# Kernel optimization log

Measured on AMD Instinct MI355X. Metric: run time of the kernel, lower is better.

The kernel has to match this reference:

```python
import jax, jax.numpy as jnp
import numpy as np

B, S, D = 16, 4096, 64


def setup_inputs() -> dict:
    key = jax.random.key(0)
    kq, kk, kv = jax.random.split(key, 3)
    q = jax.random.normal(kq, (B, S, D), dtype=jnp.float32)
    k = jax.random.normal(kk, (B, S, D), dtype=jnp.float32)
    v = jax.random.normal(kv, (B, S, D), dtype=jnp.float32)
    inv_scale_factor = jnp.float32(1.0 / np.sqrt(D))  # source DIVIDES by this
    p = 0  # dropout prob (deterministic baseline -> identity)
    return {"q": q, "k": k, "v": v, "inv_scale_factor": inv_scale_factor, "p": p}


def reference(q, k, v, inv_scale_factor, p):
    # qk = q @ k^T ; scaled = qk / inv_scale_factor (faithful to source)
    scores = jnp.einsum("bsd,btd->bst", q, k) / inv_scale_factor  # [B,S,S]
    attn = jax.nn.softmax(scores, axis=-1)
    # dropout with p=0 is identity (eval-mode baseline)
    out = jnp.einsum("bst,btd->bsd", attn, v)  # [B,S,D]
    return out
```

## Files before the change

### kernel.cpp

```cpp
#include <hip/hip_runtime.h>
#include <hip/hip_bf16.h>

typedef float f32x4 __attribute__((ext_vector_type(4)));
typedef float f32x16 __attribute__((ext_vector_type(16)));
typedef _Float16 half8 __attribute__((ext_vector_type(8)));
typedef __bf16 bf16x8 __attribute__((ext_vector_type(8)));
typedef __bf16 bf16x4 __attribute__((ext_vector_type(4)));
typedef unsigned short ushort_t;

constexpr int Bb = 16, Ss = 4096, Dd = 64;
constexpr int KBLK = 32, QBLK = 128;
constexpr int NT = Ss / KBLK;
constexpr float kLOG2E = 1.44269504088896340736f;
constexpr float DEFER_THR = 10.0f;

constexpr int KP_BLOCKS = (Bb * Ss * Dd / 8) / 256;
constexpr int VT_BLOCKS = (Bb * Dd * (Ss / 32)) / 256;

#define GLOAD_LDS16(gp, lp)                                                              \
    __builtin_amdgcn_global_load_lds(                                                    \
        (const __attribute__((address_space(1))) void*)(gp),                             \
        (__attribute__((address_space(3))) void*)(lp), 16, 0, 0)

__global__ __launch_bounds__(256)
void prep_f16s(const float* __restrict__ K, const float* __restrict__ V,
               _Float16* __restrict__ Khi, _Float16* __restrict__ Klo,
               _Float16* __restrict__ Vt)
{
    const int bid = blockIdx.x;
    if (bid < KP_BLOCKS) {
        const size_t idx = ((size_t)bid * 256 + threadIdx.x) * 8;
        const float4 a = *reinterpret_cast<const float4*>(K + idx);
        const float4 c = *reinterpret_cast<const float4*>(K + idx + 4);
        float xs[8] = {a.x, a.y, a.z, a.w, c.x, c.y, c.z, c.w};
        half8 h8, l8;
#pragma unroll
        for (int i = 0; i < 8; ++i) {
            const _Float16 h = (_Float16)xs[i];
            h8[i] = h;
            l8[i] = (_Float16)(xs[i] - (float)h);
        }
        *reinterpret_cast<half8*>(Khi + idx) = h8;
        *reinterpret_cast<half8*>(Klo + idx) = l8;
    } else {
        const int t = (bid - KP_BLOCKS) * 256 + threadIdx.x;
        const int d = t & 63;
        const int s32 = (t >> 6) & (Ss / 32 - 1);
        const int b = t >> 13;
        const float* vp = V + ((size_t)b * Ss + (size_t)s32 * 32) * Dd + d;
        __align__(16) _Float16 ob[32];
#pragma unroll
        for (int j = 0; j < 32; ++j) ob[j] = (_Float16)vp[(size_t)j * Dd];
        _Float16* op = Vt + ((size_t)b * Dd + d) * Ss + (size_t)s32 * 32;
#pragma unroll
        for (int j8 = 0; j8 < 4; ++j8)
            *reinterpret_cast<half8*>(op + j8 * 8) = *reinterpret_cast<half8*>(ob + j8 * 8);
    }
}

__global__ __launch_bounds__(512, 4)
void attn_fwd_v5(const float* __restrict__ Q, const float* __restrict__ inv_scale,
                 const _Float16* __restrict__ Khi, const _Float16* __restrict__ Klo,
                 const _Float16* __restrict__ Vt, float* __restrict__ Out)
{
    __shared__ __align__(16) unsigned char smem[48 * 1024];

    const int tid = threadIdx.x;
    const int lane = tid & 63;
    const int w = tid >> 6;
    const int p = w & 1;
    const int qg = w >> 1;
    const int l31 = lane & 31;
    const int hi = lane >> 5;

    const int bid = (blockIdx.x & 7) * 64 + (blockIdx.x >> 3);
    const int b = bid >> 5;
    const int q0 = (bid & 31) * QBLK;

    const _Float16* KhB = Khi + (size_t)b * Ss * Dd;
    const _Float16* KlB = Klo + (size_t)b * Ss * Dd;
    const _Float16* VB = Vt + (size_t)b * Dd * Ss;

    const int c = tid & 255;
    const int kk = c >> 3;
    const int ksrc = kk * Dd + (((c & 7) ^ (kk & 7)) << 3);
    const int dd_ = c >> 2;
    const size_t vsrc = (size_t)dd_ * Ss + (((c & 3) ^ (dd_ & 3)) << 3);

#define STAGE(t)                                                                            \
    do {                                                                                    \
        const int _sl = (t) & 3;                                                            \
        if (tid < 256) {                                                                    \
            GLOAD_LDS16(KhB + (size_t)(t) * (KBLK * Dd) + ksrc,                             \
                        smem + _sl * 4096 + c * 16);                                        \
            GLOAD_LDS16(KlB + (size_t)(t) * (KBLK * Dd) + ksrc,                             \
                        smem + 16384 + _sl * 4096 + c * 16);                                \
        } else {                                                                            \
            GLOAD_LDS16(VB + (size_t)(t) * KBLK + vsrc,                                     \
                        smem + 32768 + _sl * 4096 + c * 16);                                \
        }                                                                                   \
    } while (0)

    STAGE(0);
    STAGE(1);

    int koff[4], voff[4];
#pragma unroll
    for (int ks = 0; ks < 4; ++ks)
        koff[ks] = l31 * 128 + ((((ks << 1) + hi) ^ (l31 & 7)) << 4);
#pragma unroll
    for (int i = 0; i < 4; ++i) {
        const int d = (i >> 1) * 32 + l31;
        voff[i] = d * 64 + (((((i & 1) << 1) + hi) ^ (d & 3)) << 4);
    }

    union H8 { half8 h; unsigned int u[4]; };
    H8 qhi[4], qlo[4];
    {
        const float s2 = (1.0f / inv_scale[0]) * kLOG2E;
        const float* qrow = Q + ((size_t)b * Ss + q0 + qg * 32 + l31) * Dd;
#pragma unroll
        for (int ks = 0; ks < 4; ++ks) {
            const int d0 = ks * 16 + hi * 8;
            const float4 a = *reinterpret_cast<const float4*>(qrow + d0);
            const float4 cc = *reinterpret_cast<const float4*>(qrow + d0 + 4);
            float xs[8] = {a.x, a.y, a.z, a.w, cc.x, cc.y, cc.z, cc.w};
#pragma unroll
            for (int i = 0; i < 8; ++i) {
                const float x = xs[i] * s2;
                const _Float16 h = (_Float16)x;
                qhi[ks].h[i] = h;
                qlo[ks].h[i] = (_Float16)(x - (float)h);
            }
        }
    }

    f32x16 O0, O1;
#pragma unroll
    for (int r = 0; r < 16; ++r) { O0[r] = 0.f; O1[r] = 0.f; }
    float m_run = -INFINITY, l_run = 0.f;

    __syncthreads();

    for (int it = 0; it < NT / 2; ++it) {
        const int t = 2 * it + p;
        const unsigned char* khbase = smem + (t & 3) * 4096;
        const unsigned char* klbase = smem + 16384 + (t & 3) * 4096;
        const unsigned char* vbase = smem + 32768 + (t & 3) * 4096;

        if (it < NT / 2 - 1) { STAGE(2 * it + 2); STAGE(2 * it + 3); }

        f32x16 S;
#pragma unroll
        for (int r = 0; r < 16; ++r) S[r] = 0.f;
#pragma unroll
        for (int ks = 0; ks < 4; ++ks) {
            const half8 kh = *reinterpret_cast<const half8*>(khbase + koff[ks]);
            const half8 kl = *reinterpret_cast<const half8*>(klbase + koff[ks]);
            S = __builtin_amdgcn_mfma_f32_32x32x16_f16(kh, qhi[ks].h, S, 0, 0, 0);
            S = __builtin_amdgcn_mfma_f32_32x32x16_f16(kl, qhi[ks].h, S, 0, 0, 0);
            S = __builtin_amdgcn_mfma_f32_32x32x16_f16(kh, qlo[ks].h, S, 0, 0, 0);
        }

        float tmax = S[0];
#pragma unroll
        for (int r = 1; r < 16; ++r) tmax = fmaxf(tmax, S[r]);
        tmax = fmaxf(tmax, __shfl_xor(tmax, 32));

        float fac = 1.0f;
        if (__any(tmax > m_run + DEFER_THR)) {
            const float m_new = fmaxf(m_run, tmax);
            fac = __builtin_amdgcn_exp2f(m_run - m_new);
            m_run = m_new;
#pragma unroll
            for (int r = 0; r < 16; ++r) { O0[r] *= fac; O1[r] *= fac; }
        }

        float tsum = 0.f;
#pragma unroll
        for (int r = 0; r < 16; ++r) {
            S[r] = __builtin_amdgcn_exp2f(S[r] - m_run);
            tsum += S[r];
        }
        tsum += __shfl_xor(tsum, 32);
        l_run = l_run * fac + tsum;

        unsigned int wd[8];
#pragma unroll
        for (int j = 0; j < 8; ++j) {
            const auto h2 = __builtin_amdgcn_cvt_pkrtz(S[2 * j], S[2 * j + 1]);
            wd[j] = __builtin_bit_cast(unsigned int, h2);
        }
        auto xhalf = [&](unsigned int& a, unsigned int& cx) {
            const unsigned int y = hi ? a : cx;
            const unsigned int sy = __shfl_xor(y, 32);
            const unsigned int na = hi ? sy : a;
            const unsigned int nc = hi ? cx : sy;
            a = na; cx = nc;
        };
        xhalf(wd[0], wd[2]);
        xhalf(wd[1], wd[3]);
        xhalf(wd[4], wd[6]);
        xhalf(wd[5], wd[7]);

        H8 pf0, pf1;
        pf0.u[0] = wd[0]; pf0.u[1] = wd[1]; pf0.u[2] = wd[2]; pf0.u[3] = wd[3];
        pf1.u[0] = wd[4]; pf1.u[1] = wd[5]; pf1.u[2] = wd[6]; pf1.u[3] = wd[7];

        O0 = __builtin_amdgcn_mfma_f32_32x32x16_f16(
            *reinterpret_cast<const half8*>(vbase + voff[0]), pf0.h, O0, 0, 0, 0);
        O0 = __builtin_amdgcn_mfma_f32_32x32x16_f16(
            *reinterpret_cast<const half8*>(vbase + voff[1]), pf1.h, O0, 0, 0, 0);
        O1 = __builtin_amdgcn_mfma_f32_32x32x16_f16(
            *reinterpret_cast<const half8*>(vbase + voff[2]), pf0.h, O1, 0, 0, 0);
        O1 = __builtin_amdgcn_mfma_f32_32x32x16_f16(
            *reinterpret_cast<const half8*>(vbase + voff[3]), pf1.h, O1, 0, 0, 0);

        __syncthreads();
    }

    float* mO = (float*)smem;
    float* ml = (float*)(smem + 32768);

    if (p == 1) {
#pragma unroll
        for (int dblk = 0; dblk < 2; ++dblk)
#pragma unroll
            for (int rr = 0; rr < 4; ++rr) {
                f32x4 v;
                if (dblk == 0) {
                    v[0] = O0[rr * 4 + 0]; v[1] = O0[rr * 4 + 1];
                    v[2] = O0[rr * 4 + 2]; v[3] = O0[rr * 4 + 3];
                } else {
                    v[0] = O1[rr * 4 + 0]; v[1] = O1[rr * 4 + 1];
                    v[2] = O1[rr * 4 + 2]; v[3] = O1[rr * 4 + 3];
                }
                *reinterpret_cast<f32x4*>(mO + (((qg * 2 + dblk) * 4 + rr) << 8) + lane * 4) = v;
            }
        if (hi == 0) {
            ml[qg * 64 + l31] = m_run;
            ml[qg * 64 + 32 + l31] = l_run;
        }
    }
    __syncthreads();
    if (p == 0) {
        const float m1 = ml[qg * 64 + l31];
        const float l1 = ml[qg * 64 + 32 + l31];
        const float mm = fmaxf(m_run, m1);
        float f0 = __builtin_amdgcn_exp2f(m_run - mm);
        float f1 = __builtin_amdgcn_exp2f(m1 - mm);
        const float inv = 1.0f / (l_run * f0 + l1 * f1);
        f0 *= inv; f1 *= inv;
        float* orow = Out + ((size_t)b * Ss + q0 + qg * 32 + l31) * Dd;
#pragma unroll
        for (int dblk = 0; dblk < 2; ++dblk)
#pragma unroll
            for (int rr = 0; rr < 4; ++rr) {
                const f32x4 ov = *reinterpret_cast<const f32x4*>(
                    mO + (((qg * 2 + dblk) * 4 + rr) << 8) + lane * 4);
                f32x4 res;
#pragma unroll
                for (int j = 0; j < 4; ++j) {
                    const float mine = (dblk == 0) ? O0[rr * 4 + j] : O1[rr * 4 + j];
                    res[j] = mine * f0 + ov[j] * f1;
                }
                *reinterpret_cast<f32x4*>(orow + dblk * 32 + rr * 8 + hi * 4) = res;
            }
    }
#undef STAGE
}

__global__ __launch_bounds__(256)
void attn_fwd_fallback(const float* __restrict__ Q, const float* __restrict__ K,
                       const float* __restrict__ V, const float* __restrict__ inv_scale,
                       float* __restrict__ Out)
{
    __shared__ __align__(16) ushort_t sKhi[KBLK * Dd];
    __shared__ __align__(16) ushort_t sKlo[KBLK * Dd];
    __shared__ __align__(16) ushort_t sVt[Dd * KBLK];
    __shared__ __align__(16) ushort_t sP[4][16 * KBLK];

    const int tid = threadIdx.x;
    const int lane = tid & 63;
    const int w = tid >> 6;
    const int q15 = lane & 15;
    const int g = lane >> 4;
    const int b = blockIdx.x >> 6;
    const int q0 = (blockIdx.x & 63) * 64;
    const float scale = 1.0f / inv_scale[0];

    const float* qptr = Q + (((size_t)b * Ss) + q0 + w * 16 + q15) * Dd;
    bf16x8 qhi[2], qlo[2];
#pragma unroll
    for (int ds = 0; ds < 2; ++ds) {
        const float4 f0 = *reinterpret_cast<const float4*>(qptr + ds * 32 + g * 8);
        const float4 f1 = *reinterpret_cast<const float4*>(qptr + ds * 32 + g * 8 + 4);
        float xs[8] = {f0.x, f0.y, f0.z, f0.w, f1.x, f1.y, f1.z, f1.w};
#pragma unroll
        for (int i = 0; i < 8; ++i) {
            __bf16 h = (__bf16)xs[i];
            qhi[ds][i] = h;
            qlo[ds][i] = (__bf16)(xs[i] - (float)h);
        }
    }
    const int krs = tid >> 3;
    const int kc8 = (tid & 7) * 8;
    const int kidx = krs * Dd + (kc8 ^ ((krs & 7) << 3));
    const float* kbase = K + ((size_t)b * Ss) * Dd;
    const int vd = tid & 63;
    const int vk8 = (tid >> 6) * 8;
    const int vidx = vd * KBLK + (vk8 ^ ((vd & 3) << 3));
    const float* vbase = V + ((size_t)b * Ss) * Dd;

    f32x4 Oacc[4];
#pragma unroll
    for (int dt = 0; dt < 4; ++dt)
#pragma unroll
        for (int r = 0; r < 4; ++r) Oacc[dt][r] = 0.f;
    float m_run = -INFINITY, l_run = 0.f;

    for (int k0 = 0; k0 < Ss; k0 += KBLK) {
        {
            const float* p0 = kbase + (size_t)(k0 + krs) * Dd + kc8;
            const float4 a = *reinterpret_cast<const float4*>(p0);
            const float4 c = *reinterpret_cast<const float4*>(p0 + 4);
            float xs[8] = {a.x, a.y, a.z, a.w, c.x, c.y, c.z, c.w};
            bf16x8 h8, l8;
#pragma unroll
            for (int i = 0; i < 8; ++i) {
                __bf16 h = (__bf16)xs[i];
                h8[i] = h;
                l8[i] = (__bf16)(xs[i] - (float)h);
            }
            *reinterpret_cast<bf16x8*>(&sKhi[kidx]) = h8;
            *reinterpret_cast<bf16x8*>(&sKlo[kidx]) = l8;
        }
        {
            bf16x8 v8;
#pragma unroll
            for (int j = 0; j < 8; ++j) v8[j] = (__bf16)vbase[(size_t)(k0 + vk8 + j) * Dd + vd];
            *reinterpret_cast<bf16x8*>(&sVt[vidx]) = v8;
        }
        __syncthreads();

        float z[2][4];
#pragma unroll
        for (int t = 0; t < 2; ++t) {
            const int krow = t * 16 + q15;
            f32x4 acc;
            acc[0] = acc[1] = acc[2] = acc[3] = 0.f;
#pragma unroll
            for (int ds = 0; ds < 2; ++ds) {
                const int ci = (ds * 32 + g * 8) ^ ((krow & 7) << 3);
                const bf16x8 kh = *reinterpret_cast<const bf16x8*>(&sKhi[krow * Dd + ci]);
                const bf16x8 kl = *reinterpret_cast<const bf16x8*>(&sKlo[krow * Dd + ci]);
                acc = __builtin_amdgcn_mfma_f32_16x16x32_bf16(kh, qhi[ds], acc, 0, 0, 0);
                acc = __builtin_amdgcn_mfma_f32_16x16x32_bf16(kl, qhi[ds], acc, 0, 0, 0);
                acc = __builtin_amdgcn_mfma_f32_16x16x32_bf16(kh, qlo[ds], acc, 0, 0, 0);
            }
#pragma unroll
            for (int r = 0; r < 4; ++r) z[t][r] = acc[r] * scale;
        }

        float tmax = z[0][0];
#pragma unroll
        for (int t = 0; t < 2; ++t)
#pragma unroll
            for (int r = 0; r < 4; ++r) tmax = fmaxf(tmax, z[t][r]);
        tmax = fmaxf(tmax, __shfl_xor(tmax, 16));
        tmax = fmaxf(tmax, __shfl_xor(tmax, 32));
        const float m_new = fmaxf(m_run, tmax);

        float pz[2][4];
        float tsum = 0.f;
#pragma unroll
        for (int t = 0; t < 2; ++t)
#pragma unroll
            for (int r = 0; r < 4; ++r) {
                const float e = __builtin_amdgcn_exp2f((z[t][r] - m_new) * kLOG2E);
                pz[t][r] = e;
                tsum += e;
            }
        tsum += __shfl_xor(tsum, 16);
        tsum += __shfl_xor(tsum, 32);
        const float fac = __builtin_amdgcn_exp2f((m_run - m_new) * kLOG2E);
        l_run = l_run * fac + tsum;
        m_run = m_new;

#pragma unroll
        for (int t = 0; t < 2; ++t) {
            bf16x4 pb;
#pragma unroll
            for (int r = 0; r < 4; ++r) pb[r] = (__bf16)pz[t][r];
            const int pidx = q15 * KBLK + ((t * 16 + g * 4) ^ ((q15 & 3) << 3));
            *reinterpret_cast<bf16x4*>(&sP[w][pidx]) = pb;
        }
        {
            const float fr0 = __shfl(fac, g * 4 + 0);
            const float fr1 = __shfl(fac, g * 4 + 1);
            const float fr2 = __shfl(fac, g * 4 + 2);
            const float fr3 = __shfl(fac, g * 4 + 3);
#pragma unroll
            for (int dt = 0; dt < 4; ++dt) {
                Oacc[dt][0] *= fr0; Oacc[dt][1] *= fr1;
                Oacc[dt][2] *= fr2; Oacc[dt][3] *= fr3;
            }
        }
        const int paidx = q15 * KBLK + ((g * 8) ^ ((q15 & 3) << 3));
        const bf16x8 pa = *reinterpret_cast<const bf16x8*>(&sP[w][paidx]);
#pragma unroll
        for (int dt = 0; dt < 4; ++dt) {
            const int dd = dt * 16 + q15;
            const bf16x8 vf =
                *reinterpret_cast<const bf16x8*>(&sVt[dd * KBLK + ((g * 8) ^ ((dd & 3) << 3))]);
            Oacc[dt] = __builtin_amdgcn_mfma_f32_16x16x32_bf16(pa, vf, Oacc[dt], 0, 0, 0);
        }
        __syncthreads();
    }

    const float invl = 1.0f / l_run;
    float il[4];
#pragma unroll
    for (int r = 0; r < 4; ++r) il[r] = __shfl(invl, g * 4 + r);
    float* obase = Out + (((size_t)b * Ss) + q0 + w * 16) * Dd;
#pragma unroll
    for (int dt = 0; dt < 4; ++dt)
#pragma unroll
        for (int r = 0; r < 4; ++r)
            obase[(size_t)(g * 4 + r) * Dd + dt * 16 + q15] = Oacc[dt][r] * il[r];
}

extern "C" void kernel_launch(void* const* d_in, const int* in_sizes, int n_in,
                              void* d_out, int out_size, void* d_ws, size_t ws_size,
                              hipStream_t stream)
{
    const float* q = (const float*)d_in[0];
    const float* k = (const float*)d_in[1];
    const float* v = (const float*)d_in[2];
    const float* inv_scale = (const float*)d_in[3];
    float* out = (float*)d_out;
    (void)in_sizes; (void)n_in; (void)out_size;

    const size_t NKV = (size_t)Bb * Ss * Dd;
    const size_t need = NKV * 3 * sizeof(_Float16);

    if (ws_size >= need) {
        _Float16* Khi = (_Float16*)d_ws;
        _Float16* Klo = Khi + NKV;
        _Float16* Vt = Klo + NKV;
        hipLaunchKernelGGL(prep_f16s, dim3(KP_BLOCKS + VT_BLOCKS), dim3(256), 0, stream,
                           k, v, Khi, Klo, Vt);
        hipLaunchKernelGGL(attn_fwd_v5, dim3(Bb * (Ss / QBLK)), dim3(512), 0, stream,
                           q, inv_scale, Khi, Klo, Vt, out);
    } else {
        hipLaunchKernelGGL(attn_fwd_fallback, dim3(Bb * 64), dim3(256), 0, stream,
                           q, k, v, inv_scale, out);
    }
}
```

Baseline: 170.5 us.

## Software-pipeline QK^T of next tile with softmax and PV of previous tile

Restructures the main loop so each iteration issues the QK^T MFMAs for the next key tile into one score buffer while running softmax and PV on the previous tile's scores held in a second buffer. V staging grows to eight LDS slots (64 KB shared memory) so V stays resident one tile longer, and the V swizzle is changed to a different XOR pattern. It also raises wave priority around the MFMA sections. The aim is to hide exp/shuffle latency behind matrix work, at the cost of more registers and more LDS, which may reduce occupancy.

Measured after the change: 178.4 us. +4.7%, slower.

```diff
diff --git a/kernel.cpp b/kernel.cpp
--- a/kernel.cpp
+++ b/kernel.cpp
@@ -58,12 +58,14 @@
     }
 }
 
+union H8 { half8 h; unsigned int u[4]; };
+
 __global__ __launch_bounds__(512, 4)
-void attn_fwd_v5(const float* __restrict__ Q, const float* __restrict__ inv_scale,
+void attn_fwd_v6(const float* __restrict__ Q, const float* __restrict__ inv_scale,
                  const _Float16* __restrict__ Khi, const _Float16* __restrict__ Klo,
                  const _Float16* __restrict__ Vt, float* __restrict__ Out)
 {
-    __shared__ __align__(16) unsigned char smem[48 * 1024];
+    __shared__ __align__(16) unsigned char smem[64 * 1024];
 
     const int tid = threadIdx.x;
     const int lane = tid & 63;
@@ -85,19 +87,18 @@
     const int kk = c >> 3;
     const int ksrc = kk * Dd + (((c & 7) ^ (kk & 7)) << 3);
     const int dd_ = c >> 2;
-    const size_t vsrc = (size_t)dd_ * Ss + (((c & 3) ^ (dd_ & 3)) << 3);
+    const size_t vsrc = (size_t)dd_ * Ss + (((c & 3) ^ ((dd_ >> 1) & 3)) << 3);
 
 #define STAGE(t)                                                                            \
     do {                                                                                    \
-        const int _sl = (t) & 3;                                                            \
         if (tid < 256) {                                                                    \
             GLOAD_LDS16(KhB + (size_t)(t) * (KBLK * Dd) + ksrc,                             \
-                        smem + _sl * 4096 + c * 16);                                        \
+                        smem + ((t) & 3) * 4096 + c * 16);                                  \
             GLOAD_LDS16(KlB + (size_t)(t) * (KBLK * Dd) + ksrc,                             \
-                        smem + 16384 + _sl * 4096 + c * 16);                                \
+                        smem + 16384 + ((t) & 3) * 4096 + c * 16);                          \
         } else {                                                                            \
             GLOAD_LDS16(VB + (size_t)(t) * KBLK + vsrc,                                     \
-                        smem + 32768 + _sl * 4096 + c * 16);                                \
+                        smem + 32768 + ((t) & 7) * 4096 + c * 16);                          \
         }                                                                                   \
     } while (0)
 
@@ -111,10 +112,9 @@
 #pragma unroll
     for (int i = 0; i < 4; ++i) {
         const int d = (i >> 1) * 32 + l31;
-        voff[i] = d * 64 + (((((i & 1) << 1) + hi) ^ (d & 3)) << 4);
-    }
-
-    union H8 { half8 h; unsigned int u[4]; };
+        voff[i] = d * 64 + (((((i & 1) << 1) + hi) ^ ((d >> 1) & 3)) << 4);
+    }
+
     H8 qhi[4], qlo[4];
     {
         const float s2 = (1.0f / inv_scale[0]) * kLOG2E;
@@ -135,89 +135,103 @@
         }
     }
 
-    f32x16 O0, O1;
-#pragma unroll
-    for (int r = 0; r < 16; ++r) { O0[r] = 0.f; O1[r] = 0.f; }
+    f32x16 Sa, Sb, O0, O1;
+#pragma unroll
+    for (int r = 0; r < 16; ++r) { O0[r] = 0.f; O1[r] = 0.f; Sa[r] = 0.f; Sb[r] = 0.f; }
     float m_run = -INFINITY, l_run = 0.f;
 
+    auto xhalf = [&](unsigned int& a, unsigned int& cx) {
+        const unsigned int y = hi ? a : cx;
+        const unsigned int sy = __shfl_xor(y, 32);
+        const unsigned int na = hi ? sy : a;
+        const unsigned int nc = hi ? cx : sy;
+        a = na; cx = nc;
+    };
+
+#define QK_STEP(IT, SQK)                                                                   \
+    do {                                                                                   \
+        const int _tq = 2 * (IT) + p;                                                      \
+        const unsigned char* _khb = smem + (_tq & 3) * 4096;                               \
+        const unsigned char* _klb = smem + 16384 + (_tq & 3) * 4096;                       \
+        _Pragma("unroll") for (int r = 0; r < 16; ++r) SQK[r] = 0.f;                       \
+        __builtin_amdgcn_s_setprio(1);                                                     \
+        _Pragma("unroll") for (int ks = 0; ks < 4; ++ks) {                                 \
+            const half8 _kh = *reinterpret_cast<const half8*>(_khb + koff[ks]);            \
+            const half8 _kl = *reinterpret_cast<const half8*>(_klb + koff[ks]);            \
+            SQK = __builtin_amdgcn_mfma_f32_32x32x16_f16(_kh, qhi[ks].h, SQK, 0, 0, 0);    \
+            SQK = __builtin_amdgcn_mfma_f32_32x32x16_f16(_kl, qhi[ks].h, SQK, 0, 0, 0);    \
+            SQK = __builtin_amdgcn_mfma_f32_32x32x16_f16(_kh, qlo[ks].h, SQK, 0, 0, 0);    \
+        }                                                                                  \
+        __builtin_amdgcn_s_setprio(0);                                                     \
+    } while (0)
+
+#define SM_PV(TP, SSM)                                                                     \
+    do {                                                                                   \
+        float _tmax = SSM[0];                                                              \
+        _Pragma("unroll") for (int r = 1; r < 16; ++r) _tmax = fmaxf(_tmax, SSM[r]);       \
+        _tmax = fmaxf(_tmax, __shfl_xor(_tmax, 32));                                       \
+        float _fac = 1.0f;                                                                 \
+        if (__any(_tmax > m_run + DEFER_THR)) {                                            \
+            const float _mn = fmaxf(m_run, _tmax);                                         \
+            _fac = __builtin_amdgcn_exp2f(m_run - _mn);                                    \
+            m_run = _mn;                                                                   \
+            _Pragma("unroll") for (int r = 0; r < 16; ++r) { O0[r] *= _fac; O1[r] *= _fac; } \
+        }                                                                                  \
+        float _tsum = 0.f;                                                                 \
+        _Pragma("unroll") for (int r = 0; r < 16; ++r) {                                   \
+            SSM[r] = __builtin_amdgcn_exp2f(SSM[r] - m_run);                               \
+            _tsum += SSM[r];                                                               \
+        }                                                                                  \
+        _tsum += __shfl_xor(_tsum, 32);                                                    \
+        l_run = l_run * _fac + _tsum;                                                      \
+        unsigned int _wd[8];                                                               \
+        _Pragma("unroll") for (int j = 0; j < 8; ++j) {                                    \
+            const auto _h2 = __builtin_amdgcn_cvt_pkrtz(SSM[2 * j], SSM[2 * j + 1]);       \
+            _wd[j] = __builtin_bit_cast(unsigned int, _h2);                                \
+        }                                                                                  \
+        xhalf(_wd[0], _wd[2]); xhalf(_wd[1], _wd[3]);                                      \
+        xhalf(_wd[4], _wd[6]); xhalf(_wd[5], _wd[7]);                                      \
+        H8 _pf0, _pf1;                                                                     \
+        _pf0.u[0] = _wd[0]; _pf0.u[1] = _wd[1]; _pf0.u[2] = _wd[2]; _pf0.u[3] = _wd[3];    \
+        _pf1.u[0] = _wd[4]; _pf1.u[1] = _wd[5]; _pf1.u[2] = _wd[6]; _pf1.u[3] = _wd[7];    \
+        const unsigned char* _vb = smem + 32768 + ((TP) & 7) * 4096;                       \
+        __builtin_amdgcn_s_setprio(1);                                                     \
+        O0 = __builtin_amdgcn_mfma_f32_32x32x16_f16(                                       \
+            *reinterpret_cast<const half8*>(_vb + voff[0]), _pf0.h, O0, 0, 0, 0);          \
+        O0 = __builtin_amdgcn_mfma_f32_32x32x16_f16(                                       \
+            *reinterpret_cast<const half8*>(_vb + voff[1]), _pf1.h, O0, 0, 0, 0);          \
+        O1 = __builtin_amdgcn_mfma_f32_32x32x16_f16(                                       \
+            *reinterpret_cast<const half8*>(_vb + voff[2]), _pf0.h, O1, 0, 0, 0);          \
+        O1 = __builtin_amdgcn_mfma_f32_32x32x16_f16(                                       \
+            *reinterpret_cast<const half8*>(_vb + voff[3]), _pf1.h, O1, 0, 0, 0);          \
+        __builtin_amdgcn_s_setprio(0);                                                     \
+    } while (0)
+
     __syncthreads();
 
-    for (int it = 0; it < NT / 2; ++it) {
-        const int t = 2 * it + p;
-        const unsigned char* khbase = smem + (t & 3) * 4096;
-        const unsigned char* klbase = smem + 16384 + (t & 3) * 4096;
-        const unsigned char* vbase = smem + 32768 + (t & 3) * 4096;
-
-        if (it < NT / 2 - 1) { STAGE(2 * it + 2); STAGE(2 * it + 3); }
-
-        f32x16 S;
-#pragma unroll
-        for (int r = 0; r < 16; ++r) S[r] = 0.f;
-#pragma unroll
-        for (int ks = 0; ks < 4; ++ks) {
-            const half8 kh = *reinterpret_cast<const half8*>(khbase + koff[ks]);
-            const half8 kl = *reinterpret_cast<const half8*>(klbase + koff[ks]);
-            S = __builtin_amdgcn_mfma_f32_32x32x16_f16(kh, qhi[ks].h, S, 0, 0, 0);
-            S = __builtin_amdgcn_mfma_f32_32x32x16_f16(kl, qhi[ks].h, S, 0, 0, 0);
-            S = __builtin_amdgcn_mfma_f32_32x32x16_f16(kh, qlo[ks].h, S, 0, 0, 0);
-        }
-
-        float tmax = S[0];
-#pragma unroll
-        for (int r = 1; r < 16; ++r) tmax = fmaxf(tmax, S[r]);
-        tmax = fmaxf(tmax, __shfl_xor(tmax, 32));
-
-        float fac = 1.0f;
-        if (__any(tmax > m_run + DEFER_THR)) {
-            const float m_new = fmaxf(m_run, tmax);
-            fac = __builtin_amdgcn_exp2f(m_run - m_new);
-            m_run = m_new;
-#pragma unroll
-            for (int r = 0; r < 16; ++r) { O0[r] *= fac; O1[r] *= fac; }
-        }
-
-        float tsum = 0.f;
-#pragma unroll
-        for (int r = 0; r < 16; ++r) {
-            S[r] = __builtin_amdgcn_exp2f(S[r] - m_run);
-            tsum += S[r];
-        }
-        tsum += __shfl_xor(tsum, 32);
-        l_run = l_run * fac + tsum;
-
-        unsigned int wd[8];
-#pragma unroll
-        for (int j = 0; j < 8; ++j) {
-            const auto h2 = __builtin_amdgcn_cvt_pkrtz(S[2 * j], S[2 * j + 1]);
-            wd[j] = __builtin_bit_cast(unsigned int, h2);
-        }
-        auto xhalf = [&](unsigned int& a, unsigned int& cx) {
-            const unsigned int y = hi ? a : cx;
-            const unsigned int sy = __shfl_xor(y, 32);
-            const unsigned int na = hi ? sy : a;
-            const unsigned int nc = hi ? cx : sy;
-            a = na; cx = nc;
-        };
-        xhalf(wd[0], wd[2]);
-        xhalf(wd[1], wd[3]);
-        xhalf(wd[4], wd[6]);
-        xhalf(wd[5], wd[7]);
-
-        H8 pf0, pf1;
-        pf0.u[0] = wd[0]; pf0.u[1] = wd[1]; pf0.u[2] = wd[2]; pf0.u[3] = wd[3];
-        pf1.u[0] = wd[4]; pf1.u[1] = wd[5]; pf1.u[2] = wd[6]; pf1.u[3] = wd[7];
-
-        O0 = __builtin_amdgcn_mfma_f32_32x32x16_f16(
-            *reinterpret_cast<const half8*>(vbase + voff[0]), pf0.h, O0, 0, 0, 0);
-        O0 = __builtin_amdgcn_mfma_f32_32x32x16_f16(
-            *reinterpret_cast<const half8*>(vbase + voff[1]), pf1.h, O0, 0, 0, 0);
-        O1 = __builtin_amdgcn_mfma_f32_32x32x16_f16(
-            *reinterpret_cast<const half8*>(vbase + voff[2]), pf0.h, O1, 0, 0, 0);
-        O1 = __builtin_amdgcn_mfma_f32_32x32x16_f16(
-            *reinterpret_cast<const half8*>(vbase + voff[3]), pf1.h, O1, 0, 0, 0);
-
+    STAGE(2); STAGE(3);
+    QK_STEP(0, Sa);
+    __syncthreads();
+
+    for (int ih = 0; ih < 31; ++ih) {
+        const int itA = 2 * ih + 1;
+        STAGE(2 * itA + 2); STAGE(2 * itA + 3);
+        QK_STEP(itA, Sb);
+        SM_PV(2 * itA - 2 + p, Sa);
         __syncthreads();
-    }
+
+        const int itB = 2 * ih + 2;
+        STAGE(2 * itB + 2); STAGE(2 * itB + 3);
+        QK_STEP(itB, Sa);
+        SM_PV(2 * itB - 2 + p, Sb);
+        __syncthreads();
+    }
+
+    QK_STEP(63, Sb);
+    SM_PV(124 + p, Sa);
+    __syncthreads();
+
+    SM_PV(126 + p, Sb);
 
     float* mO = (float*)smem;
     float* ml = (float*)(smem + 32768);
@@ -268,6 +282,8 @@
             }
     }
 #undef STAGE
+#undef QK_STEP
+#undef SM_PV
 }
 
 __global__ __launch_bounds__(256)
@@ -450,7 +466,7 @@
         _Float16* Vt = Klo + NKV;
         hipLaunchKernelGGL(prep_f16s, dim3(KP_BLOCKS + VT_BLOCKS), dim3(256), 0, stream,
                            k, v, Khi, Klo, Vt);
-        hipLaunchKernelGGL(attn_fwd_v5, dim3(Bb * (Ss / QBLK)), dim3(512), 0, stream,
+        hipLaunchKernelGGL(attn_fwd_v6, dim3(Bb * (Ss / QBLK)), dim3(512), 0, stream,
                            q, inv_scale, Khi, Klo, Vt, out);
     } else {
         hipLaunchKernelGGL(attn_fwd_fallback, dim3(Bb * 64), dim3(256), 0, stream,
```

## Give each wave two query sub-tiles to reuse K/V fragments with half the threads

Applied to the files above, without the earlier changes.

Shrinks the attention block from 512 to 256 threads. Each wave now processes two 32-row query sub-tiles, so every K and V fragment read from LDS feeds two MFMA chains instead of one, halving LDS reads per MFMA. All threads now issue the K-hi, K-lo and V async loads, the V swizzle pattern is changed, and s_setprio is raised around the MFMA bursts. The cost is doubled accumulator and score registers, which lowers occupancy, plus an epilogue merge that runs twice in sequence.

Result: slower. 175.5 us (+3.0%).

```diff
diff --git a/kernel.cpp b/kernel.cpp
--- a/kernel.cpp
+++ b/kernel.cpp
@@ -58,10 +58,12 @@
     }
 }
 
-__global__ __launch_bounds__(512, 4)
-void attn_fwd_v5(const float* __restrict__ Q, const float* __restrict__ inv_scale,
-                 const _Float16* __restrict__ Khi, const _Float16* __restrict__ Klo,
-                 const _Float16* __restrict__ Vt, float* __restrict__ Out)
+union H8 { half8 h; unsigned int u[4]; };
+
+__global__ __launch_bounds__(256, 2)
+void attn_fwd_v10(const float* __restrict__ Q, const float* __restrict__ inv_scale,
+                  const _Float16* __restrict__ Khi, const _Float16* __restrict__ Klo,
+                  const _Float16* __restrict__ Vt, float* __restrict__ Out)
 {
     __shared__ __align__(16) unsigned char smem[48 * 1024];
 
@@ -81,24 +83,19 @@
     const _Float16* KlB = Klo + (size_t)b * Ss * Dd;
     const _Float16* VB = Vt + (size_t)b * Dd * Ss;
 
-    const int c = tid & 255;
-    const int kk = c >> 3;
-    const int ksrc = kk * Dd + (((c & 7) ^ (kk & 7)) << 3);
-    const int dd_ = c >> 2;
-    const size_t vsrc = (size_t)dd_ * Ss + (((c & 3) ^ (dd_ & 3)) << 3);
+    const int kk = tid >> 3;
+    const int ksrc = kk * Dd + (((tid & 7) ^ (kk & 7)) << 3);
+    const int dd_ = tid >> 2;
+    const size_t vsrc = (size_t)dd_ * Ss + (((tid & 3) ^ ((dd_ >> 1) & 3)) << 3);
 
 #define STAGE(t)                                                                            \
     do {                                                                                    \
-        const int _sl = (t) & 3;                                                            \
-        if (tid < 256) {                                                                    \
-            GLOAD_LDS16(KhB + (size_t)(t) * (KBLK * Dd) + ksrc,                             \
-                        smem + _sl * 4096 + c * 16);                                        \
-            GLOAD_LDS16(KlB + (size_t)(t) * (KBLK * Dd) + ksrc,                             \
-                        smem + 16384 + _sl * 4096 + c * 16);                                \
-        } else {                                                                            \
-            GLOAD_LDS16(VB + (size_t)(t) * KBLK + vsrc,                                     \
-                        smem + 32768 + _sl * 4096 + c * 16);                                \
-        }                                                                                   \
+        GLOAD_LDS16(KhB + (size_t)(t) * (KBLK * Dd) + ksrc,                                 \
+                    smem + ((t) & 3) * 4096 + tid * 16);                                    \
+        GLOAD_LDS16(KlB + (size_t)(t) * (KBLK * Dd) + ksrc,                                 \
+                    smem + 16384 + ((t) & 3) * 4096 + tid * 16);                            \
+        GLOAD_LDS16(VB + (size_t)(t) * KBLK + vsrc,                                         \
+                    smem + 32768 + ((t) & 3) * 4096 + tid * 16);                            \
     } while (0)
 
     STAGE(0);
@@ -111,34 +108,45 @@
 #pragma unroll
     for (int i = 0; i < 4; ++i) {
         const int d = (i >> 1) * 32 + l31;
-        voff[i] = d * 64 + (((((i & 1) << 1) + hi) ^ (d & 3)) << 4);
-    }
-
-    union H8 { half8 h; unsigned int u[4]; };
-    H8 qhi[4], qlo[4];
+        voff[i] = d * 64 + (((((i & 1) << 1) + hi) ^ ((d >> 1) & 3)) << 4);
+    }
+
+    H8 qhi[2][4], qlo[2][4];
     {
         const float s2 = (1.0f / inv_scale[0]) * kLOG2E;
-        const float* qrow = Q + ((size_t)b * Ss + q0 + qg * 32 + l31) * Dd;
-#pragma unroll
-        for (int ks = 0; ks < 4; ++ks) {
-            const int d0 = ks * 16 + hi * 8;
-            const float4 a = *reinterpret_cast<const float4*>(qrow + d0);
-            const float4 cc = *reinterpret_cast<const float4*>(qrow + d0 + 4);
-            float xs[8] = {a.x, a.y, a.z, a.w, cc.x, cc.y, cc.z, cc.w};
-#pragma unroll
-            for (int i = 0; i < 8; ++i) {
-                const float x = xs[i] * s2;
-                const _Float16 h = (_Float16)x;
-                qhi[ks].h[i] = h;
-                qlo[ks].h[i] = (_Float16)(x - (float)h);
-            }
-        }
-    }
-
-    f32x16 O0, O1;
-#pragma unroll
-    for (int r = 0; r < 16; ++r) { O0[r] = 0.f; O1[r] = 0.f; }
-    float m_run = -INFINITY, l_run = 0.f;
+#pragma unroll
+        for (int qs = 0; qs < 2; ++qs) {
+            const float* qrow =
+                Q + ((size_t)b * Ss + q0 + qg * 64 + qs * 32 + l31) * Dd;
+#pragma unroll
+            for (int ks = 0; ks < 4; ++ks) {
+                const int d0 = ks * 16 + hi * 8;
+                const float4 a = *reinterpret_cast<const float4*>(qrow + d0);
+                const float4 cc = *reinterpret_cast<const float4*>(qrow + d0 + 4);
+                float xs[8] = {a.x, a.y, a.z, a.w, cc.x, cc.y, cc.z, cc.w};
+#pragma unroll
+                for (int i = 0; i < 8; ++i) {
+                    const float x = xs[i] * s2;
+                    const _Float16 h = (_Float16)x;
+                    qhi[qs][ks].h[i] = h;
+                    qlo[qs][ks].h[i] = (_Float16)(x - (float)h);
+                }
+            }
+        }
+    }
+
+    f32x16 O0, O1, O2, O3;
+#pragma unroll
+    for (int r = 0; r < 16; ++r) { O0[r] = 0.f; O1[r] = 0.f; O2[r] = 0.f; O3[r] = 0.f; }
+    float m0 = -INFINITY, l0 = 0.f, m1 = -INFINITY, l1 = 0.f;
+
+    auto xhalf = [&](unsigned int& a, unsigned int& cx) {
+        const unsigned int y = hi ? a : cx;
+        const unsigned int sy = __shfl_xor(y, 32);
+        const unsigned int na = hi ? sy : a;
+        const unsigned int nc = hi ? cx : sy;
+        a = na; cx = nc;
+    };
 
     __syncthreads();
 
@@ -150,123 +158,146 @@
 
         if (it < NT / 2 - 1) { STAGE(2 * it + 2); STAGE(2 * it + 3); }
 
-        f32x16 S;
-#pragma unroll
-        for (int r = 0; r < 16; ++r) S[r] = 0.f;
+        f32x16 S0, S1;
+#pragma unroll
+        for (int r = 0; r < 16; ++r) { S0[r] = 0.f; S1[r] = 0.f; }
+        __builtin_amdgcn_s_setprio(1);
 #pragma unroll
         for (int ks = 0; ks < 4; ++ks) {
             const half8 kh = *reinterpret_cast<const half8*>(khbase + koff[ks]);
             const half8 kl = *reinterpret_cast<const half8*>(klbase + koff[ks]);
-            S = __builtin_amdgcn_mfma_f32_32x32x16_f16(kh, qhi[ks].h, S, 0, 0, 0);
-            S = __builtin_amdgcn_mfma_f32_32x32x16_f16(kl, qhi[ks].h, S, 0, 0, 0);
-            S = __builtin_amdgcn_mfma_f32_32x32x16_f16(kh, qlo[ks].h, S, 0, 0, 0);
-        }
-
-        float tmax = S[0];
-#pragma unroll
-        for (int r = 1; r < 16; ++r) tmax = fmaxf(tmax, S[r]);
-        tmax = fmaxf(tmax, __shfl_xor(tmax, 32));
-
-        float fac = 1.0f;
-        if (__any(tmax > m_run + DEFER_THR)) {
-            const float m_new = fmaxf(m_run, tmax);
-            fac = __builtin_amdgcn_exp2f(m_run - m_new);
-            m_run = m_new;
-#pragma unroll
-            for (int r = 0; r < 16; ++r) { O0[r] *= fac; O1[r] *= fac; }
-        }
-
-        float tsum = 0.f;
+            S0 = __builtin_amdgcn_mfma_f32_32x32x16_f16(kh, qhi[0][ks].h, S0, 0, 0, 0);
+            S1 = __builtin_amdgcn_mfma_f32_32x32x16_f16(kh, qhi[1][ks].h, S1, 0, 0, 0);
+            S0 = __builtin_amdgcn_mfma_f32_32x32x16_f16(kl, qhi[0][ks].h, S0, 0, 0, 0);
+            S1 = __builtin_amdgcn_mfma_f32_32x32x16_f16(kl, qhi[1][ks].h, S1, 0, 0, 0);
+            S0 = __builtin_amdgcn_mfma_f32_32x32x16_f16(kh, qlo[0][ks].h, S0, 0, 0, 0);
+            S1 = __builtin_amdgcn_mfma_f32_32x32x16_f16(kh, qlo[1][ks].h, S1, 0, 0, 0);
+        }
+        __builtin_amdgcn_s_setprio(0);
+
+        float t0 = S0[0], t1 = S1[0];
+#pragma unroll
+        for (int r = 1; r < 16; ++r) { t0 = fmaxf(t0, S0[r]); t1 = fmaxf(t1, S1[r]); }
+        t0 = fmaxf(t0, __shfl_xor(t0, 32));
+        t1 = fmaxf(t1, __shfl_xor(t1, 32));
+
+        float fac0 = 1.0f, fac1 = 1.0f;
+        if (__any(fmaxf(t0 - m0, t1 - m1) > DEFER_THR)) {
+            const float mn0 = fmaxf(m0, t0);
+            fac0 = __builtin_amdgcn_exp2f(m0 - mn0);
+            m0 = mn0;
+            const float mn1 = fmaxf(m1, t1);
+            fac1 = __builtin_amdgcn_exp2f(m1 - mn1);
+            m1 = mn1;
+#pragma unroll
+            for (int r = 0; r < 16; ++r) {
+                O0[r] *= fac0; O1[r] *= fac0;
+                O2[r] *= fac1; O3[r] *= fac1;
+            }
+        }
+
+        float ts0 = 0.f, ts1 = 0.f;
 #pragma unroll
         for (int r = 0; r < 16; ++r) {
-            S[r] = __builtin_amdgcn_exp2f(S[r] - m_run);
-            tsum += S[r];
-        }
-        tsum += __shfl_xor(tsum, 32);
-        l_run = l_run * fac + tsum;
-
-        unsigned int wd[8];
+            S0[r] = __builtin_amdgcn_exp2f(S0[r] - m0);
+            ts0 += S0[r];
+            S1[r] = __builtin_amdgcn_exp2f(S1[r] - m1);
+            ts1 += S1[r];
+        }
+        ts0 += __shfl_xor(ts0, 32);
+        ts1 += __shfl_xor(ts1, 32);
+        l0 = l0 * fac0 + ts0;
+        l1 = l1 * fac1 + ts1;
+
+        unsigned int wa[8], wb[8];
 #pragma unroll
         for (int j = 0; j < 8; ++j) {
-            const auto h2 = __builtin_amdgcn_cvt_pkrtz(S[2 * j], S[2 * j + 1]);
-            wd[j] = __builtin_bit_cast(unsigned int, h2);
-        }
-        auto xhalf = [&](unsigned int& a, unsigned int& cx) {
-            const unsigned int y = hi ? a : cx;
-            const unsigned int sy = __shfl_xor(y, 32);
-            const unsigned int na = hi ? sy : a;
-            const unsigned int nc = hi ? cx : sy;
-            a = na; cx = nc;
-        };
-        xhalf(wd[0], wd[2]);
-        xhalf(wd[1], wd[3]);
-        xhalf(wd[4], wd[6]);
-        xhalf(wd[5], wd[7]);
-
-        H8 pf0, pf1;
-        pf0.u[0] = wd[0]; pf0.u[1] = wd[1]; pf0.u[2] = wd[2]; pf0.u[3] = wd[3];
-        pf1.u[0] = wd[4]; pf1.u[1] = wd[5]; pf1.u[2] = wd[6]; pf1.u[3] = wd[7];
-
-        O0 = __builtin_amdgcn_mfma_f32_32x32x16_f16(
-            *reinterpret_cast<const half8*>(vbase + voff[0]), pf0.h, O0, 0, 0, 0);
-        O0 = __builtin_amdgcn_mfma_f32_32x32x16_f16(
-            *reinterpret_cast<const half8*>(vbase + voff[1]), pf1.h, O0, 0, 0, 0);
-        O1 = __builtin_amdgcn_mfma_f32_32x32x16_f16(
-            *reinterpret_cast<const half8*>(vbase + voff[2]), pf0.h, O1, 0, 0, 0);
-        O1 = __builtin_amdgcn_mfma_f32_32x32x16_f16(
-            *reinterpret_cast<const half8*>(vbase + voff[3]), pf1.h, O1, 0, 0, 0);
+            const auto ha = __builtin_amdgcn_cvt_pkrtz(S0[2 * j], S0[2 * j + 1]);
+            wa[j] = __builtin_bit_cast(unsigned int, ha);
+            const auto hb = __builtin_amdgcn_cvt_pkrtz(S1[2 * j], S1[2 * j + 1]);
+            wb[j] = __builtin_bit_cast(unsigned int, hb);
+        }
+        xhalf(wa[0], wa[2]); xhalf(wa[1], wa[3]);
+        xhalf(wa[4], wa[6]); xhalf(wa[5], wa[7]);
+        xhalf(wb[0], wb[2]); xhalf(wb[1], wb[3]);
+        xhalf(wb[4], wb[6]); xhalf(wb[5], wb[7]);
+
+        H8 pa0, pa1, pb0, pb1;
+        pa0.u[0] = wa[0]; pa0.u[1] = wa[1]; pa0.u[2] = wa[2]; pa0.u[3] = wa[3];
+        pa1.u[0] = wa[4]; pa1.u[1] = wa[5]; pa1.u[2] = wa[6]; pa1.u[3] = wa[7];
+        pb0.u[0] = wb[0]; pb0.u[1] = wb[1]; pb0.u[2] = wb[2]; pb0.u[3] = wb[3];
+        pb1.u[0] = wb[4]; pb1.u[1] = wb[5]; pb1.u[2] = wb[6]; pb1.u[3] = wb[7];
+
+        const half8 vf0 = *reinterpret_cast<const half8*>(vbase + voff[0]);
+        const half8 vf1 = *reinterpret_cast<const half8*>(vbase + voff[1]);
+        const half8 vf2 = *reinterpret_cast<const half8*>(vbase + voff[2]);
+        const half8 vf3 = *reinterpret_cast<const half8*>(vbase + voff[3]);
+        __builtin_amdgcn_s_setprio(1);
+        O0 = __builtin_amdgcn_mfma_f32_32x32x16_f16(vf0, pa0.h, O0, 0, 0, 0);
+        O2 = __builtin_amdgcn_mfma_f32_32x32x16_f16(vf0, pb0.h, O2, 0, 0, 0);
+        O0 = __builtin_amdgcn_mfma_f32_32x32x16_f16(vf1, pa1.h, O0, 0, 0, 0);
+        O2 = __builtin_amdgcn_mfma_f32_32x32x16_f16(vf1, pb1.h, O2, 0, 0, 0);
+        O1 = __builtin_amdgcn_mfma_f32_32x32x16_f16(vf2, pa0.h, O1, 0, 0, 0);
+        O3 = __builtin_amdgcn_mfma_f32_32x32x16_f16(vf2, pb0.h, O3, 0, 0, 0);
+        O1 = __builtin_amdgcn_mfma_f32_32x32x16_f16(vf3, pa1.h, O1, 0, 0, 0);
+        O3 = __builtin_amdgcn_mfma_f32_32x32x16_f16(vf3, pb1.h, O3, 0, 0, 0);
+        __builtin_amdgcn_s_setprio(0);
 
         __syncthreads();
     }
 
     float* mO = (float*)smem;
-    float* ml = (float*)(smem + 32768);
-
-    if (p == 1) {
-#pragma unroll
-        for (int dblk = 0; dblk < 2; ++dblk)
-#pragma unroll
-            for (int rr = 0; rr < 4; ++rr) {
-                f32x4 v;
-                if (dblk == 0) {
-                    v[0] = O0[rr * 4 + 0]; v[1] = O0[rr * 4 + 1];
-                    v[2] = O0[rr * 4 + 2]; v[3] = O0[rr * 4 + 3];
-                } else {
-                    v[0] = O1[rr * 4 + 0]; v[1] = O1[rr * 4 + 1];
-                    v[2] = O1[rr * 4 + 2]; v[3] = O1[rr * 4 + 3];
-                }
-                *reinterpret_cast<f32x4*>(mO + (((qg * 2 + dblk) * 4 + rr) << 8) + lane * 4) = v;
-            }
-        if (hi == 0) {
-            ml[qg * 64 + l31] = m_run;
-            ml[qg * 64 + 32 + l31] = l_run;
-        }
-    }
-    __syncthreads();
-    if (p == 0) {
-        const float m1 = ml[qg * 64 + l31];
-        const float l1 = ml[qg * 64 + 32 + l31];
-        const float mm = fmaxf(m_run, m1);
-        float f0 = __builtin_amdgcn_exp2f(m_run - mm);
-        float f1 = __builtin_amdgcn_exp2f(m1 - mm);
-        const float inv = 1.0f / (l_run * f0 + l1 * f1);
-        f0 *= inv; f1 *= inv;
-        float* orow = Out + ((size_t)b * Ss + q0 + qg * 32 + l31) * Dd;
-#pragma unroll
-        for (int dblk = 0; dblk < 2; ++dblk)
-#pragma unroll
-            for (int rr = 0; rr < 4; ++rr) {
-                const f32x4 ov = *reinterpret_cast<const f32x4*>(
-                    mO + (((qg * 2 + dblk) * 4 + rr) << 8) + lane * 4);
-                f32x4 res;
-#pragma unroll
-                for (int j = 0; j < 4; ++j) {
-                    const float mine = (dblk == 0) ? O0[rr * 4 + j] : O1[rr * 4 + j];
-                    res[j] = mine * f0 + ov[j] * f1;
-                }
-                *reinterpret_cast<f32x4*>(orow + dblk * 32 + rr * 8 + hi * 4) = res;
-            }
-    }
+    float* ml = (float*)(smem + 16384);
+
+#define MERGE_ROUND(OA, OB, MV, LV, QS)                                                     \
+    do {                                                                                    \
+        if (p == 1) {                                                                       \
+            _Pragma("unroll") for (int rr = 0; rr < 4; ++rr) {                              \
+                f32x4 va, vb;                                                               \
+                _Pragma("unroll") for (int j = 0; j < 4; ++j) {                             \
+                    va[j] = OA[rr * 4 + j];                                                 \
+                    vb[j] = OB[rr * 4 + j];                                                 \
+                }                                                                           \
+                *reinterpret_cast<f32x4*>(mO + (((qg * 2 + 0) * 4 + rr) << 8) + lane * 4) = \
+                    va;                                                                     \
+                *reinterpret_cast<f32x4*>(mO + (((qg * 2 + 1) * 4 + rr) << 8) + lane * 4) = \
+                    vb;                                                                     \
+            }                                                                               \
+            if (hi == 0) {                                                                  \
+                ml[qg * 64 + l31] = MV;                                                     \
+                ml[qg * 64 + 32 + l31] = LV;                                                \
+            }                                                                               \
+        }                                                                                   \
+        __syncthreads();                                                                    \
+        if (p == 0) {                                                                       \
+            const float m_o = ml[qg * 64 + l31];                                            \
+            const float l_o = ml[qg * 64 + 32 + l31];                                       \
+            const float mm = fmaxf(MV, m_o);                                                \
+            float f0 = __builtin_amdgcn_exp2f(MV - mm);                                     \
+            float f1 = __builtin_amdgcn_exp2f(m_o - mm);                                    \
+            const float inv = 1.0f / (LV * f0 + l_o * f1);                                  \
+            f0 *= inv; f1 *= inv;                                                           \
+            float* orow = Out + ((size_t)b * Ss + q0 + qg * 64 + (QS) * 32 + l31) * Dd;     \
+            _Pragma("unroll") for (int dblk = 0; dblk < 2; ++dblk) {                        \
+                _Pragma("unroll") for (int rr = 0; rr < 4; ++rr) {                          \
+                    const f32x4 ov = *reinterpret_cast<const f32x4*>(                       \
+                        mO + (((qg * 2 + dblk) * 4 + rr) << 8) + lane * 4);                 \
+                    f32x4 res;                                                              \
+                    _Pragma("unroll") for (int j = 0; j < 4; ++j) {                         \
+                        const float mine =                                                  \
+                            (dblk == 0) ? OA[rr * 4 + j] : OB[rr * 4 + j];                  \
+                        res[j] = mine * f0 + ov[j] * f1;                                    \
+                    }                                                                       \
+                    *reinterpret_cast<f32x4*>(orow + dblk * 32 + rr * 8 + hi * 4) = res;    \
+                }                                                                           \
+            }                                                                               \
+        }                                                                                   \
+        __syncthreads();                                                                    \
+    } while (0)
+
+    MERGE_ROUND(O0, O1, m0, l0, 0);
+    MERGE_ROUND(O2, O3, m1, l1, 1);
+#undef MERGE_ROUND
 #undef STAGE
 }
 
@@ -450,7 +481,7 @@
         _Float16* Vt = Klo + NKV;
         hipLaunchKernelGGL(prep_f16s, dim3(KP_BLOCKS + VT_BLOCKS), dim3(256), 0, stream,
                            k, v, Khi, Klo, Vt);
-        hipLaunchKernelGGL(attn_fwd_v5, dim3(Bb * (Ss / QBLK)), dim3(512), 0, stream,
+        hipLaunchKernelGGL(attn_fwd_v10, dim3(Bb * (Ss / QBLK)), dim3(256), 0, stream,
                            q, inv_scale, Khi, Klo, Vt, out);
     } else {
         hipLaunchKernelGGL(attn_fwd_fallback, dim3(Bb * 64), dim3(256), 0, stream,
```
